# Performance work log

Measured on AMD Instinct MI355X. Metric: run time of the kernel, lower is better.

The kernel has to match this reference:

```python
import jax, jax.numpy as jnp
import numpy as np

B, H, V, L, M, D, C = 64, 512, 50000, 400, 128, 64, 64
HC = 2 * D + M + 4  # controller LSTM hidden size (one head)
EPS = 1e-8


def _lstm_step(x, h, c, Wih, Whh, bih, bhh):
    g = x @ Wih.T + bih + h @ Whh.T + bhh
    i, f, gg, o = jnp.split(g, 4, axis=-1)
    c2 = jax.nn.sigmoid(f) * c + jax.nn.sigmoid(i) * jnp.tanh(gg)
    return jax.nn.sigmoid(o) * jnp.tanh(c2), c2


def _head_params(hc):
    # slices exactly as in LSTMMemoryController (k=0, single head)
    keys = hc[:, :M]                               # [B, M]
    kstr = jnp.exp(hc[:, D:D + 1])                 # [B, 1]
    gate = jax.nn.sigmoid(hc[:, D + 1:D + 2])      # [B, 1]
    erase = jax.nn.sigmoid(hc[:, D + 4:M + D + 4]) # [B, M]
    add = jax.nn.sigmoid(hc[:, 2 * D + 4:M + 2 * D + 4])  # [B, M]
    return keys, kstr, gate, erase, add


def _addressing(keys, kstr, gate, heads, memory):
    # torch cosine_similarity(keys.unsqueeze(2), memory, dim=2):
    # keys [B,M] broadcast along memory_dim D
    num = keys * memory.sum(-1)                                   # [B, M]
    nk = jnp.maximum(jnp.abs(keys) * jnp.sqrt(jnp.float32(D)), EPS)
    nm = jnp.maximum(jnp.linalg.norm(memory, axis=-1), EPS)
    cos = num / (nk * nm)
    content = jax.nn.softmax(kstr * cos, axis=1)                  # [B, M]
    # faithful to original: heads[k] indexes axis 0 (k=0) -> shape [1, M]
    gated = gate * content + (1.0 - gate) * heads[0]
    return gated[:, None, :]                                      # [B, 1, M]


def reference(input_ids, h0, c0, encoder_outputs, word_occurrence_indicator,
              coverage, memory, read_heads, write_heads,
              read_h, read_c, write_h, write_c,
              emb, attn_W, attn_b, cov_W, state_W, comb_W, comb_b,
              rpre_W, rpre_b, wpre_W, wpre_b,
              r_Wih, r_Whh, r_bih, r_bhh,
              w_Wih, w_Whh, w_bih, w_bhh,
              l_Wih, l_Whh, l_bih, l_bhh,
              out_W, out_b):
    embedded = emb[input_ids]                                     # [B, H]
    ia = jnp.concatenate([embedded, h0], 1) @ attn_W.T + attn_b  # [B, L]
    tc = (coverage + ia) @ cov_W.T
    ts = c0 @ state_W.T
    aw = jax.nn.softmax(tc + ia + ts, axis=1)                     # [B, L]
    attn_applied = jnp.einsum('bl,blh->bh', aw, encoder_outputs)  # [B, H]
    out0 = jnp.concatenate([embedded, attn_applied], 1) @ comb_W.T + comb_b  # [B, H]

    hm = jnp.concatenate([h0, memory.reshape(-1, M * D)], 1)
    rh, rc = _lstm_step(hm @ rpre_W.T + rpre_b, read_h, read_c, r_Wih, r_Whh, r_bih, r_bhh)
    wh, wc = _lstm_step(hm @ wpre_W.T + wpre_b, write_h, write_c, w_Wih, w_Whh, w_bih, w_bhh)
    rk, rks, rg, _, _ = _head_params(rh)
    wk, wks, wg, we, wa = _head_params(wh)
    rw = _addressing(rk, rks, rg, read_heads, memory)             # [B, 1, M]
    ww = _addressing(wk, wks, wg, write_heads, memory)            # [B, 1, M]

    read_in = jnp.einsum('bkm,bmd->bkd', rw, memory).reshape(-1, D)
    h1, c1 = _lstm_step(jnp.concatenate([out0, read_in], 1), h0, c0,
                        l_Wih, l_Whh, l_bih, l_bhh)
    # residual (h1 + out0) is computed in the original but unused by its output path

    w0 = ww[:, 0, :, None]                                        # [B, M, 1]
    new_memory = memory * (1.0 - w0 * we[:, :, None]) + w0 * wa[:, :, None]
    new_coverage = coverage + ia

    log_probs = jax.nn.log_softmax(c1[:, None, :] @ out_W.T + out_b, axis=-1)  # [B, 1, V]
    return log_probs, h1, c1, new_memory, new_coverage


def setup_inputs() -> dict:
    key = jax.random.key(0)
    ks = iter(jax.random.split(key, 48))

    def rn(shape, fan_in):
        return jax.random.normal(next(ks), shape, jnp.float32) / np.sqrt(fan_in)

    inp = {
        'input_ids': jax.random.randint(next(ks), (B,), 0, V),
        'h0': jax.random.normal(next(ks), (B, H), jnp.float32),
        'c0': jax.random.normal(next(ks), (B, H), jnp.float32),
        'encoder_outputs': jax.random.normal(next(ks), (B, L, H), jnp.float32),
        'word_occurrence_indicator': jnp.zeros((B, L), jnp.float32),
        'coverage': jnp.zeros((B, L), jnp.float32),
        'memory': jax.random.normal(next(ks), (B, M, D), jnp.float32),
        'read_heads': jnp.zeros((B, 1, M), jnp.float32),
        'write_heads': jnp.zeros((B, 1, M), jnp.float32),
        'read_h': jnp.zeros((B, HC), jnp.float32),
        'read_c': jnp.zeros((B, HC), jnp.float32),
        'write_h': jnp.zeros((B, HC), jnp.float32),
        'write_c': jnp.zeros((B, HC), jnp.float32),
        'emb': rn((V, H), H),
        'attn_W': rn((L, 2 * H), 2 * H), 'attn_b': jnp.zeros((L,), jnp.float32),
        'cov_W': rn((L, L), L),
        'state_W': rn((L, H), H),
        'comb_W': rn((H, 2 * H), 2 * H), 'comb_b': jnp.zeros((H,), jnp.float32),
        'rpre_W': rn((C, M * D + H), M * D + H), 'rpre_b': jnp.zeros((C,), jnp.float32),
        'wpre_W': rn((C, M * D + H), M * D + H), 'wpre_b': jnp.zeros((C,), jnp.float32),
        'r_Wih': rn((4 * HC, C), C), 'r_Whh': rn((4 * HC, HC), HC),
        'r_bih': jnp.zeros((4 * HC,), jnp.float32), 'r_bhh': jnp.zeros((4 * HC,), jnp.float32),
        'w_Wih': rn((4 * HC, C), C), 'w_Whh': rn((4 * HC, HC), HC),
        'w_bih': jnp.zeros((4 * HC,), jnp.float32), 'w_bhh': jnp.zeros((4 * HC,), jnp.float32),
        'l_Wih': rn((4 * H, H + D), H + D), 'l_Whh': rn((4 * H, H), H),
        'l_bih': jnp.zeros((4 * H,), jnp.float32), 'l_bhh': jnp.zeros((4 * H,), jnp.float32),
        'out_W': rn((V, H), H), 'out_b': jnp.zeros((V,), jnp.float32),
    }
    return inp
```

## Files before the change

### kernel.cpp

```cpp
#include <hip/hip_runtime.h>
#include <math.h>

#define BB 64
#define HH 512
#define VV 50000
#define LL 400
#define MM 128
#define DD 64
#define HC 260
#define EPSF 1e-8f

typedef __attribute__((ext_vector_type(8))) short bf16x8;
typedef __attribute__((ext_vector_type(4))) float f32x4;

__device__ __forceinline__ float sigmoidf(float x){ return 1.0f/(1.0f+expf(-x)); }
__device__ __forceinline__ unsigned short bf16_rne(float f){
  unsigned u = __float_as_uint(f);
  return (unsigned short)((u + 0x7fffu + ((u >> 16) & 1u)) >> 16);
}
__device__ __forceinline__ float wave_max(float v){
  #pragma unroll
  for(int o=32;o;o>>=1) v = fmaxf(v, __shfl_xor(v,o));
  return v;
}
__device__ __forceinline__ float wave_sum(float v){
  #pragma unroll
  for(int o=32;o;o>>=1) v += __shfl_xor(v,o);
  return v;
}

__global__ void k_embed(const int* __restrict__ ids, const float* __restrict__ emb,
                        const float* __restrict__ h0, float* __restrict__ xcat1,
                        float* __restrict__ xcat2){
  int idx = blockIdx.x*256 + threadIdx.x;
  if (idx >= BB*HH) return;
  int b = idx >> 9, h = idx & 511;
  float e = emb[(long)ids[b]*HH + h];
  xcat1[b*1024 + h] = e;
  xcat2[b*1024 + h] = e;
  xcat1[b*1024 + 512 + h] = h0[idx];
}

template<int NB, int FUSE>
__global__ __launch_bounds__(256) void k_gemv(const float* __restrict__ A,
                                              const float* __restrict__ A2,
                                              const float* __restrict__ W,
                                              const float* __restrict__ b1,
                                              float* __restrict__ C,
                                              int K, int N, int ldc){
  int b = blockIdx.y;
  int wid = threadIdx.x >> 6, lane = threadIdx.x & 63;
  int n = blockIdx.x*4 + wid;
  if (n >= N) return;
  const float4* A4  = (const float4*)(A + (long)b*K);
  const float4* A24 = (const float4*)(A2 + (long)b*K);
  const float4* W4  = (const float4*)(W + (long)n*K);
  int K4 = K >> 2;
  float acc = 0.f;
  for (int k = lane; k < K4; k += 64){
    float4 a = A4[k];
    if (FUSE){ float4 a2 = A24[k]; a.x+=a2.x; a.y+=a2.y; a.z+=a2.z; a.w+=a2.w; }
    float4 w = W4[k];
    acc += a.x*w.x + a.y*w.y + a.z*w.z + a.w*w.w;
  }
  acc = wave_sum(acc);
  if (lane == 0){
    if (NB) acc += b1[n];
    C[(long)b*ldc + n] = acc;
  }
}

__global__ void k_cov(const float* __restrict__ cov, const float* __restrict__ ia,
                      float* __restrict__ out){
  int idx = blockIdx.x*256 + threadIdx.x;
  if (idx >= BB*LL) return;
  out[idx] = cov[idx] + ia[idx];
}

__global__ __launch_bounds__(256) void k_softmax_aw(const float* __restrict__ ia,
                                                    const float* __restrict__ ts,
                                                    const float* __restrict__ tc,
                                                    float* __restrict__ aw){
  int b = blockIdx.x, t = threadIdx.x;
  int i0 = t, i1 = t + 256;
  float x0 = ia[b*LL+i0] + ts[b*LL+i0] + tc[b*LL+i0];
  float x1 = (i1 < LL) ? (ia[b*LL+i1] + ts[b*LL+i1] + tc[b*LL+i1]) : -INFINITY;
  __shared__ float sm[4], ss[4];
  float m = wave_max(fmaxf(x0, x1));
  if ((t & 63) == 0) sm[t>>6] = m;
  __syncthreads();
  m = fmaxf(fmaxf(sm[0], sm[1]), fmaxf(sm[2], sm[3]));
  float e0 = expf(x0 - m);
  float e1 = (i1 < LL) ? expf(x1 - m) : 0.0f;
  float s = wave_sum(e0 + e1);
  if ((t & 63) == 0) ss[t>>6] = s;
  __syncthreads();
  float tot = ss[0] + ss[1] + ss[2] + ss[3];
  float inv = 1.0f / tot;
  aw[b*LL + i0] = e0 * inv;
  if (i1 < LL) aw[b*LL + i1] = e1 * inv;
}

__global__ __launch_bounds__(256) void k_attn_part(const float* __restrict__ aw,
                                                   const float* __restrict__ enc,
                                                   float* __restrict__ part){
  int b = blockIdx.x, lc = blockIdx.y, t = threadIdx.x;
  const float* awb = aw + b*LL + lc*25;
  const float* eb  = enc + ((long)b*LL + lc*25)*HH;
  float a0 = 0.f, a1 = 0.f;
  for (int l = 0; l < 25; l++){
    float a = awb[l];
    a0 += a * eb[(long)l*HH + t];
    a1 += a * eb[(long)l*HH + t + 256];
  }
  part[((b*16 + lc) << 9) + t]       = a0;
  part[((b*16 + lc) << 9) + t + 256] = a1;
}

__global__ void k_attn_reduce(const float* __restrict__ part, float* __restrict__ xcat2){
  int idx = blockIdx.x*256 + threadIdx.x;
  if (idx >= BB*HH) return;
  int b = idx >> 9, h = idx & 511;
  float s = 0.f;
  #pragma unroll
  for (int lc = 0; lc < 16; lc++) s += part[((b*16 + lc) << 9) + h];
  xcat2[b*1024 + 512 + h] = s;
}

__global__ __launch_bounds__(256) void k_pre_gemv(const float* __restrict__ h0,
                                                  const float* __restrict__ mem,
                                                  const float* __restrict__ rW,
                                                  const float* __restrict__ wW,
                                                  float* __restrict__ part){
  int wid = threadIdx.x >> 6, lane = threadIdx.x & 63;
  int n = blockIdx.x*4 + wid;
  int b = blockIdx.y;
  int z = blockIdx.z;
  int which = z >> 3, chunk = z & 7;
  const float* W = which ? wW : rW;
  const float4* W4 = (const float4*)(W + (long)n*8704 + chunk*1088);
  const float4* H4 = (const float4*)(h0 + (long)b*HH);
  const float4* M4 = (const float4*)(mem + (long)b*8192 + (chunk*1088 - 512));
  float acc = 0.f;
  #pragma unroll
  for (int i = 0; i < 5; i++){
    int k4 = lane + i*64;
    if (k4 < 272){
      int kg4 = chunk*272 + k4;
      float4 a = (kg4 < 128) ? H4[kg4] : M4[k4];
      float4 w = W4[k4];
      acc += a.x*w.x + a.y*w.y + a.z*w.z + a.w*w.w;
    }
  }
  acc = wave_sum(acc);
  if (lane == 0) part[z*4096 + b*64 + n] = acc;
}

__global__ void k_pre_reduce(const float* __restrict__ part, const float* __restrict__ rb,
                             const float* __restrict__ wb, float* __restrict__ pre_r,
                             float* __restrict__ pre_w){
  int idx = blockIdx.x*256 + threadIdx.x;
  if (idx >= 8192) return;
  int which = idx >> 12;
  int r = idx & 4095;
  float s = 0.f;
  #pragma unroll
  for (int c = 0; c < 8; c++) s += part[((which<<3)+c)*4096 + r];
  int n = r & 63;
  s += which ? wb[n] : rb[n];
  (which ? pre_w : pre_r)[r] = s;
}

__global__ __launch_bounds__(256) void k_gates_rw(const float* __restrict__ pre_r,
    const float* __restrict__ pre_w, const float* __restrict__ read_h,
    const float* __restrict__ write_h,
    const float* __restrict__ rWih, const float* __restrict__ rWhh,
    const float* __restrict__ rbih, const float* __restrict__ rbhh,
    const float* __restrict__ wWih, const float* __restrict__ wWhh,
    const float* __restrict__ wbih, const float* __restrict__ wbhh,
    float* __restrict__ g_r, float* __restrict__ g_w){
  int which = blockIdx.z;
  int b = blockIdx.y;
  int wid = threadIdx.x >> 6, lane = threadIdx.x & 63;
  int n = blockIdx.x*4 + wid;
  const float* pre = which ? pre_w : pre_r;
  const float* hh  = which ? write_h : read_h;
  const float* Wih = which ? wWih : rWih;
  const float* Whh = which ? wWhh : rWhh;
  float acc = pre[b*64 + lane] * Wih[n*64 + lane];
  const float* hb = hh + b*HC;
  const float* wr = Whh + (long)n*HC;
  #pragma unroll
  for (int i = 0; i < 5; i++){
    int k = lane + i*64;
    if (k < HC) acc += hb[k]*wr[k];
  }
  acc = wave_sum(acc);
  if (lane == 0){
    acc += (which ? wbih : rbih)[n] + (which ? wbhh : rbhh)[n];
    (which ? g_w : g_r)[(long)b*4*HC + n] = acc;
  }
}

__global__ void k_lstm_rw(const float* __restrict__ g_r, const float* __restrict__ g_w,
                          const float* __restrict__ read_c, const float* __restrict__ write_c,
                          float* __restrict__ rh, float* __restrict__ wh){
  int idx = blockIdx.x*256 + threadIdx.x;
  if (idx >= 2*BB*HC) return;
  int which = idx >= BB*HC;
  int r = which ? idx - BB*HC : idx;
  int b = r / HC, j = r - b*HC;
  const float* g = (which ? g_w : g_r) + (long)b*4*HC;
  float c2 = sigmoidf(g[HC + j]) * (which ? write_c : read_c)[r]
           + sigmoidf(g[j]) * tanhf(g[2*HC + j]);
  (which ? wh : rh)[r] = sigmoidf(g[3*HC + j]) * tanhf(c2);
}

__global__ __launch_bounds__(128) void k_address(const float* __restrict__ rh,
                                                 const float* __restrict__ whv,
                                                 const float* __restrict__ rheads,
                                                 const float* __restrict__ wheads,
                                                 const float* __restrict__ mem,
                                                 float* __restrict__ rwout,
                                                 float* __restrict__ wwout){
  int which = blockIdx.y;
  int b = blockIdx.x, m = threadIdx.x;
  const float* hc = which ? whv : rh;
  const float* heads0 = which ? wheads : rheads;
  float* wout = which ? wwout : rwout;
  const float* mr = mem + ((long)b*MM + m)*DD;
  float s = 0.f, q = 0.f;
  #pragma unroll 8
  for (int d = 0; d < DD; d++){ float v = mr[d]; s += v; q += v*v; }
  float key  = hc[b*HC + m];
  float kstr = expf(hc[b*HC + 64]);
  float gate = sigmoidf(hc[b*HC + 65]);
  float nk = fmaxf(fabsf(key)*8.0f, EPSF);
  float nm = fmaxf(sqrtf(q), EPSF);
  float z  = kstr * (key*s) / (nk*nm);
  __shared__ float sm[2], ss[2];
  float mx = wave_max(z);
  if ((m & 63) == 0) sm[m>>6] = mx;
  __syncthreads();
  mx = fmaxf(sm[0], sm[1]);
  float e = expf(z - mx);
  float w = wave_sum(e);
  if ((m & 63) == 0) ss[m>>6] = w;
  __syncthreads();
  float content = e / (ss[0] + ss[1]);
  wout[b*MM + m] = gate*content + (1.0f - gate)*heads0[m];
}

__global__ void k_readin(const float* __restrict__ rw, const float* __restrict__ mem,
                         float* __restrict__ xcat3){
  int b = blockIdx.x, d = threadIdx.x;
  float s = 0.f;
  for (int m = 0; m < MM; m++) s += rw[b*MM + m] * mem[((long)b*MM + m)*DD + d];
  xcat3[b*576 + 512 + d] = s;
}

__global__ void k_newmem(const float* __restrict__ mem, const float* __restrict__ ww,
                         const float* __restrict__ wh, float* __restrict__ out){
  int idx = blockIdx.x*256 + threadIdx.x;
  if (idx >= BB*MM*DD) return;
  int b = idx >> 13;
  int m = (idx & 8191) >> 6;
  float w0 = ww[b*MM + m];
  float we = sigmoidf(wh[b*HC + 68 + m]);
  float wa = sigmoidf(wh[b*HC + 132 + m]);
  out[idx] = mem[idx]*(1.0f - w0*we) + w0*wa;
}

__global__ __launch_bounds__(256) void k_lstm_main(const float* __restrict__ xcat3,
                                                   const float* __restrict__ h0,
                                                   const float* __restrict__ lWih,
                                                   const float* __restrict__ lWhh,
                                                   const float* __restrict__ bih,
                                                   const float* __restrict__ bhh,
                                                   const float* __restrict__ c0,
                                                   float* __restrict__ h1,
                                                   float* __restrict__ c1,
                                                   unsigned short* __restrict__ c1b){
  int wid = threadIdx.x >> 6, lane = threadIdx.x & 63;
  int j = blockIdx.x*4 + wid;
  int b = blockIdx.y;
  const float4* A1 = (const float4*)(xcat3 + (long)b*576);
  const float4* A2 = (const float4*)(h0 + (long)b*HH);
  float gv[4];
  #pragma unroll
  for (int g = 0; g < 4; g++){
    int n = g*HH + j;
    const float4* W1 = (const float4*)(lWih + (long)n*576);
    const float4* W2 = (const float4*)(lWhh + (long)n*HH);
    float s = 0.f;
    #pragma unroll
    for (int i = 0; i < 3; i++){
      int k = lane + i*64;
      if (k < 144){ float4 a = A1[k], w = W1[k]; s += a.x*w.x + a.y*w.y + a.z*w.z + a.w*w.w; }
    }
    #pragma unroll
    for (int i = 0; i < 2; i++){
      int k = lane + i*64;
      float4 a = A2[k], w = W2[k]; s += a.x*w.x + a.y*w.y + a.z*w.z + a.w*w.w;
    }
    gv[g] = wave_sum(s);
  }
  if (lane == 0){
    #pragma unroll
    for (int g = 0; g < 4; g++){ int n = g*HH + j; gv[g] += bih[n] + bhh[n]; }
    float c2 = sigmoidf(gv[1])*c0[b*HH + j] + sigmoidf(gv[0])*tanhf(gv[2]);
    h1[b*HH + j] = sigmoidf(gv[3])*tanhf(c2);
    c1[b*HH + j] = c2;
    c1b[b*HH + j] = bf16_rne(c2);
  }
}

__global__ __launch_bounds__(256) void k_logits_mfma(const unsigned short* __restrict__ Ab,
                                                     const float* __restrict__ W,
                                                     const float* __restrict__ bias,
                                                     float* __restrict__ C){
  int wid = threadIdx.x >> 6, lane = threadIdx.x & 63;
  int strip = blockIdx.x*4 + wid;
  if (strip >= 3125) return;
  int nl = lane & 15;
  int q  = lane >> 4;
  int n  = strip*16 + nl;
  const float* wrow = W + (long)n*HH + q*8;
  const unsigned short* a0p = Ab + (0*16 + nl)*HH + q*8;
  const unsigned short* a1p = Ab + (1*16 + nl)*HH + q*8;
  const unsigned short* a2p = Ab + (2*16 + nl)*HH + q*8;
  const unsigned short* a3p = Ab + (3*16 + nl)*HH + q*8;
  f32x4 acc0 = {0.f,0.f,0.f,0.f}, acc1 = acc0, acc2 = acc0, acc3 = acc0;
  #pragma unroll 4
  for (int ks = 0; ks < 16; ks++){
    const float4* wp = (const float4*)(wrow + ks*32);
    float4 w0 = wp[0];
    float4 w1 = wp[1];
    bf16x8 bf;
    bf[0] = (short)bf16_rne(w0.x); bf[1] = (short)bf16_rne(w0.y);
    bf[2] = (short)bf16_rne(w0.z); bf[3] = (short)bf16_rne(w0.w);
    bf[4] = (short)bf16_rne(w1.x); bf[5] = (short)bf16_rne(w1.y);
    bf[6] = (short)bf16_rne(w1.z); bf[7] = (short)bf16_rne(w1.w);
    bf16x8 a0 = *(const bf16x8*)(a0p + ks*32);
    bf16x8 a1 = *(const bf16x8*)(a1p + ks*32);
    bf16x8 a2 = *(const bf16x8*)(a2p + ks*32);
    bf16x8 a3 = *(const bf16x8*)(a3p + ks*32);
    acc0 = __builtin_amdgcn_mfma_f32_16x16x32_bf16(a0, bf, acc0, 0, 0, 0);
    acc1 = __builtin_amdgcn_mfma_f32_16x16x32_bf16(a1, bf, acc1, 0, 0, 0);
    acc2 = __builtin_amdgcn_mfma_f32_16x16x32_bf16(a2, bf, acc2, 0, 0, 0);
    acc3 = __builtin_amdgcn_mfma_f32_16x16x32_bf16(a3, bf, acc3, 0, 0, 0);
  }
  float bv = bias[n];
  #pragma unroll
  for (int r = 0; r < 4; r++){
    int m = q*4 + r;
    C[(long)(m     )*VV + n] = acc0[r] + bv;
    C[(long)(m + 16)*VV + n] = acc1[r] + bv;
    C[(long)(m + 32)*VV + n] = acc2[r] + bv;
    C[(long)(m + 48)*VV + n] = acc3[r] + bv;
  }
}

__global__ __launch_bounds__(256) void k_ls1(const float* __restrict__ lp,
                                             float* __restrict__ pm, float* __restrict__ ps){
  int b = blockIdx.y, c = blockIdx.x, t = threadIdx.x;
  const float* row = lp + (long)b*VV + c*2000;
  float mx = -INFINITY;
  for (int i = t; i < 2000; i += 256) mx = fmaxf(mx, row[i]);
  __shared__ float sm[4], ss[4];
  mx = wave_max(mx);
  if ((t & 63) == 0) sm[t>>6] = mx;
  __syncthreads();
  mx = fmaxf(fmaxf(sm[0], sm[1]), fmaxf(sm[2], sm[3]));
  float s = 0.f;
  for (int i = t; i < 2000; i += 256) s += expf(row[i] - mx);
  s = wave_sum(s);
  if ((t & 63) == 0) ss[t>>6] = s;
  __syncthreads();
  if (t == 0){ pm[b*25 + c] = mx; ps[b*25 + c] = ss[0]+ss[1]+ss[2]+ss[3]; }
}

__global__ void k_ls2(const float* __restrict__ pm, const float* __restrict__ ps,
                      float* __restrict__ lse){
  int b = threadIdx.x;
  float m = -INFINITY;
  for (int c = 0; c < 25; c++) m = fmaxf(m, pm[b*25 + c]);
  float s = 0.f;
  for (int c = 0; c < 25; c++) s += ps[b*25 + c]*expf(pm[b*25 + c] - m);
  lse[b] = m + logf(s);
}

__global__ void k_ls3(float* __restrict__ lp, const float* __restrict__ lse){
  int idx = blockIdx.x*256 + threadIdx.x;
  if (idx >= BB*VV) return;
  int b = idx / VV;
  lp[idx] -= lse[b];
}

extern "C" void kernel_launch(void* const* d_in, const int* in_sizes, int n_in,
                              void* d_out, int out_size, void* d_ws, size_t ws_size,
                              hipStream_t stream) {
  const int*   ids     = (const int*)  d_in[0];
  const float* h0      = (const float*)d_in[1];
  const float* c0      = (const float*)d_in[2];
  const float* enc     = (const float*)d_in[3];
  const float* cov     = (const float*)d_in[5];
  const float* mem     = (const float*)d_in[6];
  const float* rheads  = (const float*)d_in[7];
  const float* wheads  = (const float*)d_in[8];
  const float* read_h  = (const float*)d_in[9];
  const float* read_c  = (const float*)d_in[10];
  const float* write_h = (const float*)d_in[11];
  const float* write_c = (const float*)d_in[12];
  const float* emb     = (const float*)d_in[13];
  const float* attn_W  = (const float*)d_in[14];
  const float* attn_b  = (const float*)d_in[15];
  const float* cov_W   = (const float*)d_in[16];
  const float* state_W = (const float*)d_in[17];
  const float* comb_W  = (const float*)d_in[18];
  const float* comb_b  = (const float*)d_in[19];
  const float* rpre_W  = (const float*)d_in[20];
  const float* rpre_b  = (const float*)d_in[21];
  const float* wpre_W  = (const float*)d_in[22];
  const float* wpre_b  = (const float*)d_in[23];
  const float* r_Wih   = (const float*)d_in[24];
  const float* r_Whh   = (const float*)d_in[25];
  const float* r_bih   = (const float*)d_in[26];
  const float* r_bhh   = (const float*)d_in[27];
  const float* w_Wih   = (const float*)d_in[28];
  const float* w_Whh   = (const float*)d_in[29];
  const float* w_bih   = (const float*)d_in[30];
  const float* w_bhh   = (const float*)d_in[31];
  const float* l_Wih   = (const float*)d_in[32];
  const float* l_Whh   = (const float*)d_in[33];
  const float* l_bih   = (const float*)d_in[34];
  const float* l_bhh   = (const float*)d_in[35];
  const float* out_W   = (const float*)d_in[36];
  const float* out_b   = (const float*)d_in[37];

  float* out  = (float*)d_out;
  float* lp   = out;
  float* h1   = out + 3200000;
  float* c1   = h1 + 32768;
  float* nmem = c1 + 32768;
  float* ncov = nmem + 524288;

  float* w = (float*)d_ws;
  float* xcat1 = w;
  float* xcat2 = xcat1 + 65536;
  float* xcat3 = xcat2 + 65536;
  float* ia    = xcat3 + 36864;
  float* ts    = ia + 25600;
  float* tc    = ts + 25600;
  float* aw    = tc + 25600;
  float* U     = aw + 25600;
  float* pre_r = U + 557056;
  float* pre_w = pre_r + 4096;
  float* g_r   = pre_w + 4096;
  float* g_w   = g_r + 66560;
  float* rh    = g_w + 66560;
  float* wh    = rh + 16640;
  float* rw    = wh + 16640;
  float* wwgt  = rw + 8192;
  float* pm    = wwgt + 8192;
  float* ps    = pm + 1600;
  float* lse   = ps + 1600;
  unsigned short* c1b = (unsigned short*)(lse + 64);

  k_embed<<<128, 256, 0, stream>>>(ids, emb, h0, xcat1, xcat2);
  k_gemv<1,0><<<dim3(100,64), 256, 0, stream>>>(xcat1, xcat1, attn_W, attn_b, ia, 1024, LL, LL);
  k_gemv<0,0><<<dim3(100,64), 256, 0, stream>>>(c0, c0, state_W, nullptr, ts, HH, LL, LL);
  k_cov<<<100, 256, 0, stream>>>(cov, ia, ncov);
  k_gemv<0,1><<<dim3(100,64), 256, 0, stream>>>(cov, ia, cov_W, nullptr, tc, LL, LL, LL);
  k_softmax_aw<<<64, 256, 0, stream>>>(ia, ts, tc, aw);
  k_attn_part<<<dim3(64,16), 256, 0, stream>>>(aw, enc, U);
  k_attn_reduce<<<128, 256, 0, stream>>>(U, xcat2);
  k_gemv<1,0><<<dim3(128,64), 256, 0, stream>>>(xcat2, xcat2, comb_W, comb_b, xcat3, 1024, HH, 576);

  k_pre_gemv<<<dim3(16,64,16), 256, 0, stream>>>(h0, mem, rpre_W, wpre_W, U);
  k_pre_reduce<<<32, 256, 0, stream>>>(U, rpre_b, wpre_b, pre_r, pre_w);

  k_gates_rw<<<dim3(260,64,2), 256, 0, stream>>>(pre_r, pre_w, read_h, write_h,
      r_Wih, r_Whh, r_bih, r_bhh, w_Wih, w_Whh, w_bih, w_bhh, g_r, g_w);
  k_lstm_rw<<<130, 256, 0, stream>>>(g_r, g_w, read_c, write_c, rh, wh);

  k_address<<<dim3(64,2), 128, 0, stream>>>(rh, wh, rheads, wheads, mem, rw, wwgt);
  k_readin<<<64, 64, 0, stream>>>(rw, mem, xcat3);
  k_newmem<<<2048, 256, 0, stream>>>(mem, wwgt, wh, nmem);

  k_lstm_main<<<dim3(128,64), 256, 0, stream>>>(xcat3, h0, l_Wih, l_Whh, l_bih, l_bhh,
                                                c0, h1, c1, c1b);

  k_logits_mfma<<<782, 256, 0, stream>>>(c1b, out_W, out_b, lp);
  k_ls1<<<dim3(25,64), 256, 0, stream>>>(lp, pm, ps);
  k_ls2<<<1, 64, 0, stream>>>(pm, ps, lse);
  k_ls3<<<12500, 256, 0, stream>>>(lp, lse);
}
```

Before: 505.2 us.

## Split logits MFMA across batch tiles per wave with batched load prefetch

Restructures the vocab-projection MFMA kernel so each block covers one 16-column strip and each of its four waves computes a different 16-row batch tile, launching 3125 blocks instead of 782. Loads of eight K-steps of weights and activations are issued up front before the conversions and MFMAs to raise memory-level parallelism. The intent is more waves in flight to saturate bandwidth on the weight stream. The cost is that the four waves reload and reconvert the same weight strip, relying on caches to absorb the redundancy, and register pressure rises from the prefetch arrays.

```diff
diff --git a/kernel.cpp b/kernel.cpp
--- a/kernel.cpp
+++ b/kernel.cpp
@@ -315,49 +315,45 @@
   }
 }
 
-__global__ __launch_bounds__(256) void k_logits_mfma(const unsigned short* __restrict__ Ab,
-                                                     const float* __restrict__ W,
-                                                     const float* __restrict__ bias,
-                                                     float* __restrict__ C){
-  int wid = threadIdx.x >> 6, lane = threadIdx.x & 63;
-  int strip = blockIdx.x*4 + wid;
-  if (strip >= 3125) return;
+__global__ __launch_bounds__(256, 4) void k_logits_mfma(const unsigned short* __restrict__ Ab,
+                                                        const float* __restrict__ W,
+                                                        const float* __restrict__ bias,
+                                                        float* __restrict__ C){
+  int mb = threadIdx.x >> 6, lane = threadIdx.x & 63;
+  int strip = blockIdx.x;
   int nl = lane & 15;
   int q  = lane >> 4;
   int n  = strip*16 + nl;
-  const float* wrow = W + (long)n*HH + q*8;
-  const unsigned short* a0p = Ab + (0*16 + nl)*HH + q*8;
-  const unsigned short* a1p = Ab + (1*16 + nl)*HH + q*8;
-  const unsigned short* a2p = Ab + (2*16 + nl)*HH + q*8;
-  const unsigned short* a3p = Ab + (3*16 + nl)*HH + q*8;
-  f32x4 acc0 = {0.f,0.f,0.f,0.f}, acc1 = acc0, acc2 = acc0, acc3 = acc0;
-  #pragma unroll 4
-  for (int ks = 0; ks < 16; ks++){
-    const float4* wp = (const float4*)(wrow + ks*32);
-    float4 w0 = wp[0];
-    float4 w1 = wp[1];
-    bf16x8 bf;
-    bf[0] = (short)bf16_rne(w0.x); bf[1] = (short)bf16_rne(w0.y);
-    bf[2] = (short)bf16_rne(w0.z); bf[3] = (short)bf16_rne(w0.w);
-    bf[4] = (short)bf16_rne(w1.x); bf[5] = (short)bf16_rne(w1.y);
-    bf[6] = (short)bf16_rne(w1.z); bf[7] = (short)bf16_rne(w1.w);
-    bf16x8 a0 = *(const bf16x8*)(a0p + ks*32);
-    bf16x8 a1 = *(const bf16x8*)(a1p + ks*32);
-    bf16x8 a2 = *(const bf16x8*)(a2p + ks*32);
-    bf16x8 a3 = *(const bf16x8*)(a3p + ks*32);
-    acc0 = __builtin_amdgcn_mfma_f32_16x16x32_bf16(a0, bf, acc0, 0, 0, 0);
-    acc1 = __builtin_amdgcn_mfma_f32_16x16x32_bf16(a1, bf, acc1, 0, 0, 0);
-    acc2 = __builtin_amdgcn_mfma_f32_16x16x32_bf16(a2, bf, acc2, 0, 0, 0);
-    acc3 = __builtin_amdgcn_mfma_f32_16x16x32_bf16(a3, bf, acc3, 0, 0, 0);
+  const float4*  W4 = (const float4*)(W + (long)n*HH + q*8);
+  const bf16x8*  Ap = (const bf16x8*)(Ab + (long)(mb*16 + nl)*HH + q*8);
+  f32x4 acc = {0.f,0.f,0.f,0.f};
+  #pragma unroll
+  for (int c = 0; c < 2; c++){
+    float4 wv[16];
+    bf16x8 av[8];
+    #pragma unroll
+    for (int i = 0; i < 8; i++){
+      int ks = c*8 + i;
+      wv[2*i]   = W4[ks*8];
+      wv[2*i+1] = W4[ks*8 + 1];
+      av[i]     = Ap[ks*4];
+    }
+    #pragma unroll
+    for (int i = 0; i < 8; i++){
+      float4 w0 = wv[2*i], w1 = wv[2*i+1];
+      bf16x8 bf;
+      bf[0] = (short)bf16_rne(w0.x); bf[1] = (short)bf16_rne(w0.y);
+      bf[2] = (short)bf16_rne(w0.z); bf[3] = (short)bf16_rne(w0.w);
+      bf[4] = (short)bf16_rne(w1.x); bf[5] = (short)bf16_rne(w1.y);
+      bf[6] = (short)bf16_rne(w1.z); bf[7] = (short)bf16_rne(w1.w);
+      acc = __builtin_amdgcn_mfma_f32_16x16x32_bf16(av[i], bf, acc, 0, 0, 0);
+    }
   }
   float bv = bias[n];
   #pragma unroll
   for (int r = 0; r < 4; r++){
-    int m = q*4 + r;
-    C[(long)(m     )*VV + n] = acc0[r] + bv;
-    C[(long)(m + 16)*VV + n] = acc1[r] + bv;
-    C[(long)(m + 32)*VV + n] = acc2[r] + bv;
-    C[(long)(m + 48)*VV + n] = acc3[r] + bv;
+    int m = mb*16 + q*4 + r;
+    C[(long)m*VV + n] = acc[r] + bv;
   }
 }
 
@@ -491,7 +487,7 @@
   k_lstm_main<<<dim3(128,64), 256, 0, stream>>>(xcat3, h0, l_Wih, l_Whh, l_bih, l_bhh,
                                                 c0, h1, c1, c1b);
 
-  k_logits_mfma<<<782, 256, 0, stream>>>(c1b, out_W, out_b, lp);
+  k_logits_mfma<<<3125, 256, 0, stream>>>(c1b, out_W, out_b, lp);
   k_ls1<<<dim3(25,64), 256, 0, stream>>>(lp, pm, ps);
   k_ls2<<<1, 64, 0, stream>>>(pm, ps, lse);
   k_ls3<<<12500, 256, 0, stream>>>(lp, lse);
```

Result: slower. 521.5 us (+3.2%).
